# Kernel optimization log

Measured on AMD Instinct MI355X. Metric: run time of the kernel, lower is better.

Reference implementation:

```python
import jax, jax.numpy as jnp
import numpy as np

D_ATOM, D_MODEL, H = 128, 512, 4
D_H = D_ATOM // H
D_FF = 4 * D_ATOM
EPS = 1e-5


def _ln(x, g, b):
    m = jnp.mean(x, axis=-1, keepdims=True)
    v = jnp.mean((x - m) ** 2, axis=-1, keepdims=True)
    return (x - m) / jnp.sqrt(v + EPS) * g + b


def setup_inputs() -> dict:
    key = jax.random.key(0)
    ks = jax.random.split(key, 20)
    B, N_ATOM, N_PAIRS, N_TOK = 2, 2048, 16384, 512
    c_atom = jax.random.normal(ks[0], (B, N_ATOM, D_ATOM), dtype=jnp.float32)
    p_lm = jax.random.normal(ks[1], (B, N_PAIRS, 16), dtype=jnp.float32)
    p_lm_idx = jax.random.randint(ks[2], (B, N_PAIRS, 2), 0, N_ATOM, dtype=jnp.int32)
    token_idx = jnp.sort(jax.random.randint(ks[3], (B, N_ATOM), 0, N_TOK, dtype=jnp.int32), axis=-1)
    s = 0.05
    w = lambda k, sh: jax.random.normal(k, sh, dtype=jnp.float32) * s
    return {
        'c_atom': c_atom, 'p_lm': p_lm, 'p_lm_idx': p_lm_idx,
        'token_idx': token_idx, 'n_tokens': N_TOK,
        'ln_attn_g': jnp.ones((D_ATOM,), jnp.float32), 'ln_attn_b': jnp.zeros((D_ATOM,), jnp.float32),
        'w_q': w(ks[4], (D_ATOM, D_ATOM)), 'w_k': w(ks[5], (D_ATOM, D_ATOM)),
        'w_v': w(ks[6], (D_ATOM, D_ATOM)), 'w_g': w(ks[7], (D_ATOM, D_ATOM)),
        'w_o': w(ks[8], (D_ATOM, D_ATOM)),
        'pb_w': w(ks[9], (16, H)), 'pb_b': jnp.zeros((H,), jnp.float32),
        'ln_ff_g': jnp.ones((D_ATOM,), jnp.float32), 'ln_ff_b': jnp.zeros((D_ATOM,), jnp.float32),
        'sw_w1': w(ks[10], (D_ATOM, D_FF)), 'sw_w2': w(ks[11], (D_ATOM, D_FF)),
        'sw_w3': w(ks[12], (D_FF, D_ATOM)),
        'tok_w': w(ks[13], (D_ATOM, D_MODEL)), 'tok_b': jnp.zeros((D_MODEL,), jnp.float32),
    }


def reference(c_atom, p_lm, p_lm_idx, token_idx, n_tokens,
              ln_attn_g, ln_attn_b, w_q, w_k, w_v, w_g, w_o, pb_w, pb_b,
              ln_ff_g, ln_ff_b, sw_w1, sw_w2, sw_w3, tok_w, tok_b):
    B, N, _ = c_atom.shape
    q_n = _ln(c_atom, ln_attn_g, ln_attn_b)
    Q = (q_n @ w_q).reshape(B, N, H, D_H)
    K = (q_n @ w_k).reshape(B, N, H, D_H)
    V = (q_n @ w_v).reshape(B, N, H, D_H)
    G = q_n @ w_g  # (B, N, d_atom)

    scores = jnp.einsum('bihd,bjhd->bhij', Q, K) / jnp.sqrt(jnp.float32(D_H))

    bias = p_lm @ pb_w + pb_b  # (B, P, H)
    def scat(src, dst, b_):
        return jnp.zeros((H, N, N), b_.dtype).at[:, src, dst].set(b_.T)
    pair_bias = jax.vmap(scat)(p_lm_idx[..., 0], p_lm_idx[..., 1], bias)
    scores = scores + pair_bias

    token_mask = token_idx[:, :, None] == token_idx[:, None, :]  # (B,N,N)
    scores = jnp.where(token_mask[:, None], scores, -jnp.inf)
    attn = jax.nn.softmax(scores, axis=-1)
    attn = jnp.nan_to_num(attn)

    att_out = jnp.einsum('bhij,bjhd->bihd', attn, V).reshape(B, N, D_ATOM)
    q = c_atom + jax.nn.sigmoid(G) * (att_out @ w_o)
    h = _ln(q, ln_ff_g, ln_ff_b)
    q = q + (jax.nn.silu(h @ sw_w1) * (h @ sw_w2)) @ sw_w3
    atom_feat = q @ tok_w + tok_b  # (B, N, d_model)

    seg = (token_idx + jnp.arange(B, dtype=token_idx.dtype)[:, None] * n_tokens).reshape(-1)
    sums = jax.ops.segment_sum(atom_feat.reshape(B * N, D_MODEL), seg, num_segments=B * n_tokens)
    cnts = jax.ops.segment_sum(jnp.ones((B * N,), atom_feat.dtype), seg, num_segments=B * n_tokens)
    out = sums / jnp.maximum(cnts, 1.0)[:, None]
    return out.reshape(B, n_tokens, D_MODEL)
```

## Files before the change

### kernel.cpp

```cpp
#include <hip/hip_runtime.h>
#include <hip/hip_bf16.h>
#include <math.h>

#define B_     2
#define N_     2048
#define DA     128
#define H_     4
#define DH     32
#define DFF    512
#define DM     512
#define NT     512
#define NP     16384
#define MAXL   32

typedef short bf16x8 __attribute__((ext_vector_type(8)));
typedef float f32x4  __attribute__((ext_vector_type(4)));

__device__ __forceinline__ short bf16r(float x) {
    union { float f; unsigned u; } v; v.f = x;
    unsigned r = v.u + 0x7FFFu + ((v.u >> 16) & 1u);
    return (short)(r >> 16);
}

__global__ __launch_bounds__(64) void ln_kernel(const float* __restrict__ x,
                                                const float* __restrict__ g,
                                                const float* __restrict__ b,
                                                short* __restrict__ y) {
    int row = blockIdx.x;
    int t = threadIdx.x;
    const float* xr = x + row * DA;
    float a0 = xr[t], a1 = xr[t + 64];
    float s = a0 + a1, sq = a0 * a0 + a1 * a1;
#pragma unroll
    for (int m = 32; m; m >>= 1) {
        s += __shfl_xor(s, m);
        sq += __shfl_xor(sq, m);
    }
    float mean = s * (1.f / 128.f);
    float var = sq * (1.f / 128.f) - mean * mean;
    float inv = rsqrtf(var + 1e-5f);
    y[row * DA + t]      = bf16r((a0 - mean) * inv * g[t] + b[t]);
    y[row * DA + t + 64] = bf16r((a1 - mean) * inv * g[t + 64] + b[t + 64]);
}

__global__ __launch_bounds__(1024) void hist_kernel(const int* __restrict__ tok,
                                                    int* __restrict__ cnt,
                                                    int* __restrict__ tst) {
    __shared__ int c[1024];
    __shared__ int s[1024];
    int tid = threadIdx.x;
    c[tid] = 0;
    __syncthreads();
#pragma unroll
    for (int i = 0; i < 4; i++) {
        int idx = tid + i * 1024;
        int b = idx >> 11;
        atomicAdd(&c[b * NT + tok[idx]], 1);
    }
    __syncthreads();
    int t = tid & (NT - 1);
    int v = c[tid];
    int* cur = c;
    int* alt = s;
    for (int d = 1; d < NT; d <<= 1) {
        int y = cur[tid];
        if (t >= d) y += cur[tid - d];
        alt[tid] = y;
        __syncthreads();
        int* tmp = cur; cur = alt; alt = tmp;
    }
    tst[tid] = cur[tid] - v;
    cnt[tid] = v;
}

__global__ __launch_bounds__(256) void pack_kernel(
        const float* __restrict__ wq, const float* __restrict__ wk,
        const float* __restrict__ wv, const float* __restrict__ wg,
        const float* __restrict__ wo, const float* __restrict__ w1,
        const float* __restrict__ w2, const float* __restrict__ w3,
        const float* __restrict__ tw,
        short* __restrict__ pqkvg, short* __restrict__ pwo,
        short* __restrict__ pw12, short* __restrict__ pw3,
        short* __restrict__ ptok) {
    int gid = blockIdx.x * 256 + threadIdx.x;
    int lane = gid & 63;
    int grp = gid >> 6;
    int quad = lane >> 4, nn = lane & 15;
    const float* src; short* dst; int stride;
    if (grp < 128) {
        int g = grp; int kt = g & 3, nt = g >> 2;
        int n = nt * 16 + nn;
        const float* w = (n < 128) ? wq : (n < 256) ? wk : (n < 384) ? wv : wg;
        src = w + (kt * 32 + quad * 8) * 128 + (n & 127);
        dst = pqkvg + (g * 64 + lane) * 8;
        stride = 128;
    } else if (grp < 160) {
        int g = grp - 128; int kt = g & 3, nt = g >> 2;
        src = wo + (kt * 32 + quad * 8) * 128 + nt * 16 + nn;
        dst = pwo + (g * 64 + lane) * 8;
        stride = 128;
    } else if (grp < 416) {
        int g = grp - 160; int kt = g & 3, nt = g >> 2;
        int n = nt * 16 + nn;
        src = ((n & 1) ? w2 : w1) + (kt * 32 + quad * 8) * 512 + (n >> 1);
        dst = pw12 + (g * 64 + lane) * 8;
        stride = 512;
    } else if (grp < 544) {
        int g = grp - 416; int kt = g & 15, nt = g >> 4;
        src = w3 + (kt * 32 + quad * 8) * 128 + nt * 16 + nn;
        dst = pw3 + (g * 64 + lane) * 8;
        stride = 128;
    } else {
        int g = grp - 544; int kt = g & 3, nt = g >> 2;
        src = tw + (kt * 32 + quad * 8) * 512 + nt * 16 + nn;
        dst = ptok + (g * 64 + lane) * 8;
        stride = 512;
    }
#pragma unroll
    for (int j = 0; j < 8; j++) dst[j] = bf16r(src[j * stride]);
}

template<int K>
__device__ __forceinline__ void gemm_tile(const short* __restrict__ A,
                                          const short* __restrict__ Bp,
                                          int m0, int nt0, int lane,
                                          f32x4 acc[4]) {
    constexpr int KT = K / 32;
    const short* arow = A + (m0 + (lane & 15)) * K + (lane >> 4) * 8;
    const short* bbase = Bp + ((size_t)nt0 * KT) * 512 + lane * 8;
#pragma unroll
    for (int kt = 0; kt < KT; kt++) {
        bf16x8 a = *(const bf16x8*)(arow + kt * 32);
#pragma unroll
        for (int nt = 0; nt < 4; nt++) {
            bf16x8 b = *(const bf16x8*)(bbase + (nt * KT + kt) * 512);
            acc[nt] = __builtin_amdgcn_mfma_f32_16x16x32_bf16(a, b, acc[nt], 0, 0, 0);
        }
    }
}

#define GEMM_PROLOG(KVAL, APTR, BPTR)                                  \
    int lane = threadIdx.x & 63;                                       \
    int m0 = blockIdx.x * 64 + (threadIdx.x >> 6) * 16;                \
    int nt0 = blockIdx.y * 4;                                          \
    f32x4 acc[4];                                                      \
    _Pragma("unroll") for (int i = 0; i < 4; i++)                      \
        _Pragma("unroll") for (int r = 0; r < 4; r++) acc[i][r] = 0.f; \
    gemm_tile<KVAL>(APTR, BPTR, m0, nt0, lane, acc);                   \
    int r0 = m0 + ((lane >> 4) << 2);                                  \
    int cc = lane & 15;

__global__ __launch_bounds__(256) void qkvg_mfma(const short* __restrict__ qn,
                                                 const short* __restrict__ Bp,
                                                 float* __restrict__ out) {
    GEMM_PROLOG(128, qn, Bp)
#pragma unroll
    for (int nt = 0; nt < 4; nt++) {
        int col = (nt0 + nt) * 16 + cc;
#pragma unroll
        for (int r = 0; r < 4; r++) out[(r0 + r) * 512 + col] = acc[nt][r];
    }
}

__global__ __launch_bounds__(256) void outproj_mfma(const short* __restrict__ atth,
                                                    const short* __restrict__ Bp,
                                                    const float* __restrict__ qkvg,
                                                    const float* __restrict__ c_atom,
                                                    float* __restrict__ qbuf) {
    GEMM_PROLOG(128, atth, Bp)
#pragma unroll
    for (int nt = 0; nt < 4; nt++) {
        int col = (nt0 + nt) * 16 + cc;
#pragma unroll
        for (int r = 0; r < 4; r++) {
            int row = r0 + r;
            float g = qkvg[row * 512 + 384 + col];
            float sg = 1.f / (1.f + expf(-g));
            qbuf[row * DA + col] = c_atom[row * DA + col] + sg * acc[nt][r];
        }
    }
}

__global__ __launch_bounds__(256) void ffn1_mfma(const short* __restrict__ h,
                                                 const short* __restrict__ Bp,
                                                 short* __restrict__ u) {
    GEMM_PROLOG(128, h, Bp)
#pragma unroll
    for (int nt = 0; nt < 4; nt++) {
        int col8 = (nt0 + nt) * 8 + (cc >> 1);
#pragma unroll
        for (int r = 0; r < 4; r++) {
            float v = acc[nt][r];
            float p = __shfl_xor(v, 1);
            if (!(lane & 1)) {
                float sil = v / (1.f + expf(-v));
                u[(r0 + r) * DFF + col8] = bf16r(sil * p);
            }
        }
    }
}

__global__ __launch_bounds__(256) void ffn2_mfma(const short* __restrict__ u,
                                                 const short* __restrict__ Bp,
                                                 const float* __restrict__ qbuf,
                                                 short* __restrict__ q2h) {
    GEMM_PROLOG(512, u, Bp)
#pragma unroll
    for (int nt = 0; nt < 4; nt++) {
        int col = (nt0 + nt) * 16 + cc;
#pragma unroll
        for (int r = 0; r < 4; r++) {
            int row = r0 + r;
            q2h[row * DA + col] = bf16r(qbuf[row * DA + col] + acc[nt][r]);
        }
    }
}

__global__ __launch_bounds__(256) void tokproj_mfma(const short* __restrict__ q2h,
                                                    const short* __restrict__ Bp,
                                                    const float* __restrict__ tb,
                                                    float* __restrict__ af) {
    GEMM_PROLOG(128, q2h, Bp)
#pragma unroll
    for (int nt = 0; nt < 4; nt++) {
        int col = (nt0 + nt) * 16 + cc;
        float bv = tb[col];
#pragma unroll
        for (int r = 0; r < 4; r++) af[(r0 + r) * DM + col] = acc[nt][r] + bv;
    }
}

__global__ void pair_win_kernel(const int* __restrict__ pidx,
                                const int* __restrict__ tok,
                                const int* __restrict__ tst,
                                int* __restrict__ winner) {
    int p = blockIdx.x * 256 + threadIdx.x;
    if (p >= B_ * NP) return;
    int b = p >> 14, pp = p & (NP - 1);
    int src = pidx[p * 2], dst = pidx[p * 2 + 1];
    int ts = tok[b * N_ + src], td = tok[b * N_ + dst];
    if (ts == td) {
        int jj = dst - tst[b * NT + td];
        if (jj < MAXL) atomicMax(&winner[(b * N_ + src) * MAXL + jj], pp);
    }
}

__global__ void pair_bias_kernel(const int* __restrict__ pidx,
                                 const int* __restrict__ tok,
                                 const int* __restrict__ tst,
                                 const int* __restrict__ winner,
                                 const float* __restrict__ plm,
                                 const float* __restrict__ pbw,
                                 const float* __restrict__ pbb,
                                 float* __restrict__ biasc) {
    int p = blockIdx.x * 256 + threadIdx.x;
    if (p >= B_ * NP) return;
    int b = p >> 14, pp = p & (NP - 1);
    int src = pidx[p * 2], dst = pidx[p * 2 + 1];
    int ts = tok[b * N_ + src], td = tok[b * N_ + dst];
    if (ts == td) {
        int jj = dst - tst[b * NT + td];
        if (jj < MAXL && winner[(b * N_ + src) * MAXL + jj] == pp) {
            const float* pl = plm + p * 16;
#pragma unroll
            for (int h = 0; h < H_; h++) {
                float s = pbb[h];
#pragma unroll
                for (int f = 0; f < 16; f++) s += pl[f] * pbw[f * H_ + h];
                biasc[((b * N_ + src) * MAXL + jj) * H_ + h] = s;
            }
        }
    }
}

__global__ __launch_bounds__(128) void attn_kernel(const float* __restrict__ qkvg,
                                                   const int* __restrict__ tok,
                                                   const int* __restrict__ tst,
                                                   const int* __restrict__ cnt,
                                                   const int* __restrict__ winner,
                                                   const float* __restrict__ biasc,
                                                   short* __restrict__ atth) {
    __shared__ float sc[H_][MAXL];
    int blk = blockIdx.x;
    int b = blk >> 11;
    int h = threadIdx.x >> 5, d = threadIdx.x & 31;
    int t = tok[blk];
    int start = tst[b * NT + t];
    int L = cnt[b * NT + t];
    if (L > MAXL) L = MAXL;
    float qv = qkvg[blk * 512 + h * DH + d];
    const float scale = 0.17677669529663687f;
    for (int jj = 0; jj < L; jj++) {
        int j = b * N_ + start + jj;
        float kv = qkvg[j * 512 + 128 + h * DH + d];
        float s = qv * kv;
#pragma unroll
        for (int m = 16; m; m >>= 1) s += __shfl_xor(s, m, 32);
        s *= scale;
        if (winner[blk * MAXL + jj] >= 0) s += biasc[(blk * MAXL + jj) * H_ + h];
        if (d == 0) sc[h][jj] = s;
    }
    __syncthreads();
    float mx = -1e30f;
    for (int jj = 0; jj < L; jj++) mx = fmaxf(mx, sc[h][jj]);
    float denom = 0.f, acc = 0.f;
    for (int jj = 0; jj < L; jj++) {
        float pj = expf(sc[h][jj] - mx);
        denom += pj;
        acc += pj * qkvg[(b * N_ + start + jj) * 512 + 256 + h * DH + d];
    }
    atth[blk * DA + h * DH + d] = bf16r(acc / denom);
}

__global__ __launch_bounds__(128) void segmean_kernel(const float* __restrict__ af,
                                                      const int* __restrict__ tst,
                                                      const int* __restrict__ cnt,
                                                      float* __restrict__ out) {
    int blk = blockIdx.x;
    int b = blk >> 9;
    int tid = threadIdx.x;
    int start = tst[blk], n = cnt[blk];
    float acc[4] = {0.f, 0.f, 0.f, 0.f};
    for (int a = 0; a < n; a++) {
        const float* row = af + (b * N_ + start + a) * DM;
#pragma unroll
        for (int c = 0; c < 4; c++) acc[c] += row[tid + c * 128];
    }
    float inv = 1.f / fmaxf((float)n, 1.f);
#pragma unroll
    for (int c = 0; c < 4; c++) out[(size_t)blk * DM + tid + c * 128] = acc[c] * inv;
}

extern "C" void kernel_launch(void* const* d_in, const int* in_sizes, int n_in,
                              void* d_out, int out_size, void* d_ws, size_t ws_size,
                              hipStream_t stream) {
    const float* c_atom  = (const float*)d_in[0];
    const float* p_lm    = (const float*)d_in[1];
    const int*   p_idx   = (const int*)d_in[2];
    const int*   tok     = (const int*)d_in[3];
    const float* ln_a_g  = (const float*)d_in[5];
    const float* ln_a_b  = (const float*)d_in[6];
    const float* w_q     = (const float*)d_in[7];
    const float* w_k     = (const float*)d_in[8];
    const float* w_v     = (const float*)d_in[9];
    const float* w_g     = (const float*)d_in[10];
    const float* w_o     = (const float*)d_in[11];
    const float* pb_w    = (const float*)d_in[12];
    const float* pb_b    = (const float*)d_in[13];
    const float* ln_f_g  = (const float*)d_in[14];
    const float* ln_f_b  = (const float*)d_in[15];
    const float* sw_w1   = (const float*)d_in[16];
    const float* sw_w2   = (const float*)d_in[17];
    const float* sw_w3   = (const float*)d_in[18];
    const float* tok_w   = (const float*)d_in[19];
    const float* tok_b   = (const float*)d_in[20];
    float* out = (float*)d_out;

    float* ws = (float*)d_ws;
    int*   cnt   = (int*)ws;
    int*   tst   = cnt + 1024;
    int*   win   = tst + 1024;
    short* pqkvg = (short*)(win + 131072);
    short* pwo   = pqkvg + 65536;
    short* pw12  = pwo + 16384;
    short* pw3   = pw12 + 131072;
    short* ptok  = pw3 + 65536;
    short* qnh   = ptok + 65536;
    short* atth  = qnh + 524288;
    float* qbuf  = (float*)(atth + 524288);
    float* qkvg  = qbuf + 524288;
    float* af    = qkvg + 2097152;
    short* hbufh = qnh;
    short* uh    = (short*)qkvg;
    short* q2h   = atth;
    float* bias  = af;

    hipMemsetAsync(win, 0xFF, 131072 * sizeof(int), stream);

    pack_kernel<<<168, 256, 0, stream>>>(w_q, w_k, w_v, w_g, w_o, sw_w1, sw_w2,
                                         sw_w3, tok_w,
                                         pqkvg, pwo, pw12, pw3, ptok);
    hist_kernel<<<1, 1024, 0, stream>>>(tok, cnt, tst);

    ln_kernel<<<B_ * N_, 64, 0, stream>>>(c_atom, ln_a_g, ln_a_b, qnh);
    qkvg_mfma<<<dim3(64, 8), 256, 0, stream>>>(qnh, pqkvg, qkvg);

    pair_win_kernel<<<B_ * NP / 256, 256, 0, stream>>>(p_idx, tok, tst, win);
    pair_bias_kernel<<<B_ * NP / 256, 256, 0, stream>>>(p_idx, tok, tst, win,
                                                        p_lm, pb_w, pb_b, bias);

    attn_kernel<<<B_ * N_, 128, 0, stream>>>(qkvg, tok, tst, cnt, win, bias, atth);
    outproj_mfma<<<dim3(64, 2), 256, 0, stream>>>(atth, pwo, qkvg, c_atom, qbuf);

    ln_kernel<<<B_ * N_, 64, 0, stream>>>(qbuf, ln_f_g, ln_f_b, hbufh);
    ffn1_mfma<<<dim3(64, 16), 256, 0, stream>>>(hbufh, pw12, uh);
    ffn2_mfma<<<dim3(64, 2), 256, 0, stream>>>(uh, pw3, qbuf, q2h);
    tokproj_mfma<<<dim3(64, 8), 256, 0, stream>>>(q2h, ptok, tok_b, af);

    segmean_kernel<<<B_ * NT, 128, 0, stream>>>(af, tst, cnt, out);
}
```

Baseline: 162.9 us.

## Fuse layernorms into GEMMs via LDS and compute pair bias inside attention

Both layernorm kernels are folded into the following QKVG and FFN1 GEMMs. Each block normalises 64 rows into padded LDS and then runs MFMA with more N-tiles per block (8 and 16), which cuts the grid to 256 blocks. The separate pair_bias kernel is removed: attention recomputes the 16-wide bias dot product on the fly for winning pairs. Three launches and the bf16 intermediate round-trips go away, at the cost of fewer blocks, more accumulator registers per thread, and redundant bias math repeated across the 32 lanes of each head.

Result: slower. 167.8 us (+3.0%).

```diff
diff --git a/kernel.cpp b/kernel.cpp
--- a/kernel.cpp
+++ b/kernel.cpp
@@ -12,6 +12,7 @@
 #define NT     512
 #define NP     16384
 #define MAXL   32
+#define LDSP   136
 
 typedef short bf16x8 __attribute__((ext_vector_type(8)));
 typedef float f32x4  __attribute__((ext_vector_type(4)));
@@ -20,27 +21,6 @@
     union { float f; unsigned u; } v; v.f = x;
     unsigned r = v.u + 0x7FFFu + ((v.u >> 16) & 1u);
     return (short)(r >> 16);
-}
-
-__global__ __launch_bounds__(64) void ln_kernel(const float* __restrict__ x,
-                                                const float* __restrict__ g,
-                                                const float* __restrict__ b,
-                                                short* __restrict__ y) {
-    int row = blockIdx.x;
-    int t = threadIdx.x;
-    const float* xr = x + row * DA;
-    float a0 = xr[t], a1 = xr[t + 64];
-    float s = a0 + a1, sq = a0 * a0 + a1 * a1;
-#pragma unroll
-    for (int m = 32; m; m >>= 1) {
-        s += __shfl_xor(s, m);
-        sq += __shfl_xor(sq, m);
-    }
-    float mean = s * (1.f / 128.f);
-    float var = sq * (1.f / 128.f) - mean * mean;
-    float inv = rsqrtf(var + 1e-5f);
-    y[row * DA + t]      = bf16r((a0 - mean) * inv * g[t] + b[t]);
-    y[row * DA + t + 64] = bf16r((a1 - mean) * inv * g[t + 64] + b[t + 64]);
 }
 
 __global__ __launch_bounds__(1024) void hist_kernel(const int* __restrict__ tok,
@@ -120,14 +100,63 @@
     for (int j = 0; j < 8; j++) dst[j] = bf16r(src[j * stride]);
 }
 
+__device__ __forceinline__ void ln_to_lds(const float* __restrict__ x,
+                                          const float* __restrict__ g,
+                                          const float* __restrict__ b,
+                                          short* __restrict__ lds) {
+    int t = threadIdx.x;
+    int row = t >> 2, sub = t & 3;
+    const float* xr = x + row * DA + sub * 32;
+    float4 v[8];
+    float s = 0.f, sq = 0.f;
+#pragma unroll
+    for (int i = 0; i < 8; i++) {
+        v[i] = *(const float4*)(xr + i * 4);
+        s  += v[i].x + v[i].y + v[i].z + v[i].w;
+        sq += v[i].x * v[i].x + v[i].y * v[i].y + v[i].z * v[i].z + v[i].w * v[i].w;
+    }
+    s += __shfl_xor(s, 1); sq += __shfl_xor(sq, 1);
+    s += __shfl_xor(s, 2); sq += __shfl_xor(sq, 2);
+    float mean = s * (1.f / 128.f);
+    float var = sq * (1.f / 128.f) - mean * mean;
+    float inv = rsqrtf(var + 1e-5f);
+    const float* gp = g + sub * 32;
+    const float* bp = b + sub * 32;
+    short* dst = lds + row * LDSP + sub * 32;
+#pragma unroll
+    for (int i = 0; i < 8; i++) {
+        dst[i * 4 + 0] = bf16r((v[i].x - mean) * inv * gp[i * 4 + 0] + bp[i * 4 + 0]);
+        dst[i * 4 + 1] = bf16r((v[i].y - mean) * inv * gp[i * 4 + 1] + bp[i * 4 + 1]);
+        dst[i * 4 + 2] = bf16r((v[i].z - mean) * inv * gp[i * 4 + 2] + bp[i * 4 + 2]);
+        dst[i * 4 + 3] = bf16r((v[i].w - mean) * inv * gp[i * 4 + 3] + bp[i * 4 + 3]);
+    }
+}
+
+template<int K, int NTT>
+__device__ __forceinline__ void gemm_lds(const short* __restrict__ Alds,
+                                         const short* __restrict__ Bp,
+                                         int nt0, int lane, f32x4* acc) {
+    constexpr int KT = K / 32;
+    const short* arow = Alds + (lane & 15) * LDSP + (lane >> 4) * 8;
+    const short* bbase = Bp + nt0 * KT * 512 + lane * 8;
+#pragma unroll
+    for (int kt = 0; kt < KT; kt++) {
+        bf16x8 a = *(const bf16x8*)(arow + kt * 32);
+#pragma unroll
+        for (int nt = 0; nt < NTT; nt++) {
+            bf16x8 b = *(const bf16x8*)(bbase + (nt * KT + kt) * 512);
+            acc[nt] = __builtin_amdgcn_mfma_f32_16x16x32_bf16(a, b, acc[nt], 0, 0, 0);
+        }
+    }
+}
+
 template<int K>
-__device__ __forceinline__ void gemm_tile(const short* __restrict__ A,
-                                          const short* __restrict__ Bp,
-                                          int m0, int nt0, int lane,
-                                          f32x4 acc[4]) {
+__device__ __forceinline__ void gemm_glb(const short* __restrict__ A,
+                                         const short* __restrict__ Bp,
+                                         int m0, int nt0, int lane, f32x4 acc[4]) {
     constexpr int KT = K / 32;
     const short* arow = A + (m0 + (lane & 15)) * K + (lane >> 4) * 8;
-    const short* bbase = Bp + ((size_t)nt0 * KT) * 512 + lane * 8;
+    const short* bbase = Bp + nt0 * KT * 512 + lane * 8;
 #pragma unroll
     for (int kt = 0; kt < KT; kt++) {
         bf16x8 a = *(const bf16x8*)(arow + kt * 32);
@@ -139,54 +168,56 @@
     }
 }
 
-#define GEMM_PROLOG(KVAL, APTR, BPTR)                                  \
-    int lane = threadIdx.x & 63;                                       \
-    int m0 = blockIdx.x * 64 + (threadIdx.x >> 6) * 16;                \
-    int nt0 = blockIdx.y * 4;                                          \
-    f32x4 acc[4];                                                      \
-    _Pragma("unroll") for (int i = 0; i < 4; i++)                      \
-        _Pragma("unroll") for (int r = 0; r < 4; r++) acc[i][r] = 0.f; \
-    gemm_tile<KVAL>(APTR, BPTR, m0, nt0, lane, acc);                   \
-    int r0 = m0 + ((lane >> 4) << 2);                                  \
+__global__ __launch_bounds__(256) void lnqkvg_mfma(const float* __restrict__ c_atom,
+                                                   const float* __restrict__ lg,
+                                                   const float* __restrict__ lb,
+                                                   const short* __restrict__ Bp,
+                                                   float* __restrict__ out) {
+    __shared__ short alds[64 * LDSP];
+    int base = blockIdx.x * 64;
+    ln_to_lds(c_atom + base * DA, lg, lb, alds);
+    __syncthreads();
+    int lane = threadIdx.x & 63;
+    int wave = threadIdx.x >> 6;
+    int nt0 = blockIdx.y * 8;
+    f32x4 acc[8];
+#pragma unroll
+    for (int i = 0; i < 8; i++)
+#pragma unroll
+        for (int r = 0; r < 4; r++) acc[i][r] = 0.f;
+    gemm_lds<128, 8>(alds + wave * 16 * LDSP, Bp, nt0, lane, acc);
+    int r0 = base + wave * 16 + ((lane >> 4) << 2);
     int cc = lane & 15;
-
-__global__ __launch_bounds__(256) void qkvg_mfma(const short* __restrict__ qn,
-                                                 const short* __restrict__ Bp,
-                                                 float* __restrict__ out) {
-    GEMM_PROLOG(128, qn, Bp)
-#pragma unroll
-    for (int nt = 0; nt < 4; nt++) {
+#pragma unroll
+    for (int nt = 0; nt < 8; nt++) {
         int col = (nt0 + nt) * 16 + cc;
 #pragma unroll
         for (int r = 0; r < 4; r++) out[(r0 + r) * 512 + col] = acc[nt][r];
     }
 }
 
-__global__ __launch_bounds__(256) void outproj_mfma(const short* __restrict__ atth,
-                                                    const short* __restrict__ Bp,
-                                                    const float* __restrict__ qkvg,
-                                                    const float* __restrict__ c_atom,
-                                                    float* __restrict__ qbuf) {
-    GEMM_PROLOG(128, atth, Bp)
-#pragma unroll
-    for (int nt = 0; nt < 4; nt++) {
-        int col = (nt0 + nt) * 16 + cc;
-#pragma unroll
-        for (int r = 0; r < 4; r++) {
-            int row = r0 + r;
-            float g = qkvg[row * 512 + 384 + col];
-            float sg = 1.f / (1.f + expf(-g));
-            qbuf[row * DA + col] = c_atom[row * DA + col] + sg * acc[nt][r];
-        }
-    }
-}
-
-__global__ __launch_bounds__(256) void ffn1_mfma(const short* __restrict__ h,
-                                                 const short* __restrict__ Bp,
-                                                 short* __restrict__ u) {
-    GEMM_PROLOG(128, h, Bp)
-#pragma unroll
-    for (int nt = 0; nt < 4; nt++) {
+__global__ __launch_bounds__(256) void lnffn1_mfma(const float* __restrict__ qbuf,
+                                                   const float* __restrict__ lg,
+                                                   const float* __restrict__ lb,
+                                                   const short* __restrict__ Bp,
+                                                   short* __restrict__ u) {
+    __shared__ short alds[64 * LDSP];
+    int base = blockIdx.x * 64;
+    ln_to_lds(qbuf + base * DA, lg, lb, alds);
+    __syncthreads();
+    int lane = threadIdx.x & 63;
+    int wave = threadIdx.x >> 6;
+    int nt0 = blockIdx.y * 16;
+    f32x4 acc[16];
+#pragma unroll
+    for (int i = 0; i < 16; i++)
+#pragma unroll
+        for (int r = 0; r < 4; r++) acc[i][r] = 0.f;
+    gemm_lds<128, 16>(alds + wave * 16 * LDSP, Bp, nt0, lane, acc);
+    int r0 = base + wave * 16 + ((lane >> 4) << 2);
+    int cc = lane & 15;
+#pragma unroll
+    for (int nt = 0; nt < 16; nt++) {
         int col8 = (nt0 + nt) * 8 + (cc >> 1);
 #pragma unroll
         for (int r = 0; r < 4; r++) {
@@ -200,11 +231,50 @@
     }
 }
 
+__global__ __launch_bounds__(256) void outproj_mfma(const short* __restrict__ atth,
+                                                    const short* __restrict__ Bp,
+                                                    const float* __restrict__ qkvg,
+                                                    const float* __restrict__ c_atom,
+                                                    float* __restrict__ qbuf) {
+    int lane = threadIdx.x & 63;
+    int m0 = blockIdx.x * 64 + (threadIdx.x >> 6) * 16;
+    int nt0 = blockIdx.y * 4;
+    f32x4 acc[4];
+#pragma unroll
+    for (int i = 0; i < 4; i++)
+#pragma unroll
+        for (int r = 0; r < 4; r++) acc[i][r] = 0.f;
+    gemm_glb<128>(atth, Bp, m0, nt0, lane, acc);
+    int r0 = m0 + ((lane >> 4) << 2);
+    int cc = lane & 15;
+#pragma unroll
+    for (int nt = 0; nt < 4; nt++) {
+        int col = (nt0 + nt) * 16 + cc;
+#pragma unroll
+        for (int r = 0; r < 4; r++) {
+            int row = r0 + r;
+            float g = qkvg[row * 512 + 384 + col];
+            float sg = 1.f / (1.f + expf(-g));
+            qbuf[row * DA + col] = c_atom[row * DA + col] + sg * acc[nt][r];
+        }
+    }
+}
+
 __global__ __launch_bounds__(256) void ffn2_mfma(const short* __restrict__ u,
                                                  const short* __restrict__ Bp,
                                                  const float* __restrict__ qbuf,
                                                  short* __restrict__ q2h) {
-    GEMM_PROLOG(512, u, Bp)
+    int lane = threadIdx.x & 63;
+    int m0 = blockIdx.x * 64 + (threadIdx.x >> 6) * 16;
+    int nt0 = blockIdx.y * 4;
+    f32x4 acc[4];
+#pragma unroll
+    for (int i = 0; i < 4; i++)
+#pragma unroll
+        for (int r = 0; r < 4; r++) acc[i][r] = 0.f;
+    gemm_glb<512>(u, Bp, m0, nt0, lane, acc);
+    int r0 = m0 + ((lane >> 4) << 2);
+    int cc = lane & 15;
 #pragma unroll
     for (int nt = 0; nt < 4; nt++) {
         int col = (nt0 + nt) * 16 + cc;
@@ -220,7 +290,17 @@
                                                     const short* __restrict__ Bp,
                                                     const float* __restrict__ tb,
                                                     float* __restrict__ af) {
-    GEMM_PROLOG(128, q2h, Bp)
+    int lane = threadIdx.x & 63;
+    int m0 = blockIdx.x * 64 + (threadIdx.x >> 6) * 16;
+    int nt0 = blockIdx.y * 4;
+    f32x4 acc[4];
+#pragma unroll
+    for (int i = 0; i < 4; i++)
+#pragma unroll
+        for (int r = 0; r < 4; r++) acc[i][r] = 0.f;
+    gemm_glb<128>(q2h, Bp, m0, nt0, lane, acc);
+    int r0 = m0 + ((lane >> 4) << 2);
+    int cc = lane & 15;
 #pragma unroll
     for (int nt = 0; nt < 4; nt++) {
         int col = (nt0 + nt) * 16 + cc;
@@ -245,40 +325,14 @@
     }
 }
 
-__global__ void pair_bias_kernel(const int* __restrict__ pidx,
-                                 const int* __restrict__ tok,
-                                 const int* __restrict__ tst,
-                                 const int* __restrict__ winner,
-                                 const float* __restrict__ plm,
-                                 const float* __restrict__ pbw,
-                                 const float* __restrict__ pbb,
-                                 float* __restrict__ biasc) {
-    int p = blockIdx.x * 256 + threadIdx.x;
-    if (p >= B_ * NP) return;
-    int b = p >> 14, pp = p & (NP - 1);
-    int src = pidx[p * 2], dst = pidx[p * 2 + 1];
-    int ts = tok[b * N_ + src], td = tok[b * N_ + dst];
-    if (ts == td) {
-        int jj = dst - tst[b * NT + td];
-        if (jj < MAXL && winner[(b * N_ + src) * MAXL + jj] == pp) {
-            const float* pl = plm + p * 16;
-#pragma unroll
-            for (int h = 0; h < H_; h++) {
-                float s = pbb[h];
-#pragma unroll
-                for (int f = 0; f < 16; f++) s += pl[f] * pbw[f * H_ + h];
-                biasc[((b * N_ + src) * MAXL + jj) * H_ + h] = s;
-            }
-        }
-    }
-}
-
 __global__ __launch_bounds__(128) void attn_kernel(const float* __restrict__ qkvg,
                                                    const int* __restrict__ tok,
                                                    const int* __restrict__ tst,
                                                    const int* __restrict__ cnt,
                                                    const int* __restrict__ winner,
-                                                   const float* __restrict__ biasc,
+                                                   const float* __restrict__ plm,
+                                                   const float* __restrict__ pbw,
+                                                   const float* __restrict__ pbb,
                                                    short* __restrict__ atth) {
     __shared__ float sc[H_][MAXL];
     int blk = blockIdx.x;
@@ -297,7 +351,14 @@
 #pragma unroll
         for (int m = 16; m; m >>= 1) s += __shfl_xor(s, m, 32);
         s *= scale;
-        if (winner[blk * MAXL + jj] >= 0) s += biasc[(blk * MAXL + jj) * H_ + h];
+        int pp = winner[blk * MAXL + jj];
+        if (pp >= 0) {
+            const float* pl = plm + (b * NP + pp) * 16;
+            float bsum = pbb[h];
+#pragma unroll
+            for (int f = 0; f < 16; f++) bsum += pl[f] * pbw[f * H_ + h];
+            s += bsum;
+        }
         if (d == 0) sc[h][jj] = s;
     }
     __syncthreads();
@@ -365,35 +426,28 @@
     short* pw12  = pwo + 16384;
     short* pw3   = pw12 + 131072;
     short* ptok  = pw3 + 65536;
-    short* qnh   = ptok + 65536;
-    short* atth  = qnh + 524288;
+    short* atth  = ptok + 65536;
     float* qbuf  = (float*)(atth + 524288);
     float* qkvg  = qbuf + 524288;
     float* af    = qkvg + 2097152;
-    short* hbufh = qnh;
     short* uh    = (short*)qkvg;
     short* q2h   = atth;
-    float* bias  = af;
 
     hipMemsetAsync(win, 0xFF, 131072 * sizeof(int), stream);
 
+    hist_kernel<<<1, 1024, 0, stream>>>(tok, cnt, tst);
     pack_kernel<<<168, 256, 0, stream>>>(w_q, w_k, w_v, w_g, w_o, sw_w1, sw_w2,
                                          sw_w3, tok_w,
                                          pqkvg, pwo, pw12, pw3, ptok);
-    hist_kernel<<<1, 1024, 0, stream>>>(tok, cnt, tst);
-
-    ln_kernel<<<B_ * N_, 64, 0, stream>>>(c_atom, ln_a_g, ln_a_b, qnh);
-    qkvg_mfma<<<dim3(64, 8), 256, 0, stream>>>(qnh, pqkvg, qkvg);
-
+
+    lnqkvg_mfma<<<dim3(64, 4), 256, 0, stream>>>(c_atom, ln_a_g, ln_a_b, pqkvg, qkvg);
     pair_win_kernel<<<B_ * NP / 256, 256, 0, stream>>>(p_idx, tok, tst, win);
-    pair_bias_kernel<<<B_ * NP / 256, 256, 0, stream>>>(p_idx, tok, tst, win,
-                                                        p_lm, pb_w, pb_b, bias);
-
-    attn_kernel<<<B_ * N_, 128, 0, stream>>>(qkvg, tok, tst, cnt, win, bias, atth);
+
+    attn_kernel<<<B_ * N_, 128, 0, stream>>>(qkvg, tok, tst, cnt, win,
+                                             p_lm, pb_w, pb_b, atth);
     outproj_mfma<<<dim3(64, 2), 256, 0, stream>>>(atth, pwo, qkvg, c_atom, qbuf);
 
-    ln_kernel<<<B_ * N_, 64, 0, stream>>>(qbuf, ln_f_g, ln_f_b, hbufh);
-    ffn1_mfma<<<dim3(64, 16), 256, 0, stream>>>(hbufh, pw12, uh);
+    lnffn1_mfma<<<dim3(64, 4), 256, 0, stream>>>(qbuf, ln_f_g, ln_f_b, pw12, uh);
     ffn2_mfma<<<dim3(64, 2), 256, 0, stream>>>(uh, pw3, qbuf, q2h);
     tokproj_mfma<<<dim3(64, 8), 256, 0, stream>>>(q2h, ptok, tok_b, af);
 
```
